# Performance work log

Measured on AMD Instinct MI355X. Metric: run time of the kernel, lower is better.

Reference implementation:

```python
import jax, jax.numpy as jnp
import numpy as np

N = 100000      # nodes
E = 3200000     # edges (avg degree 32)
F_IN = 512
HID = 256
CLS = 64


def _linear_init(k, fan_in, fan_out):
    lim = 1.0 / np.sqrt(fan_in)
    kw, kb = jax.random.split(k)
    W = jax.random.uniform(kw, (fan_in, fan_out), jnp.float32, -lim, lim)
    b = jax.random.uniform(kb, (fan_out,), jnp.float32, -lim, lim)
    return W, b


def setup_inputs() -> dict:
    key = jax.random.key(0)
    ks = jax.random.split(key, 8)
    x = jax.random.normal(ks[0], (N, F_IN), jnp.float32)
    edge_src = jax.random.randint(ks[1], (E,), 0, N, jnp.int32)
    off = jax.random.randint(ks[2], (E,), 1, N, jnp.int32)
    edge_dst = ((edge_src + off) % N).astype(jnp.int32)  # no self loops
    Wm0, bm0 = _linear_init(ks[3], F_IN, HID)
    Wv0, bv0 = _linear_init(ks[4], F_IN, HID)
    Wm1, bm1 = _linear_init(ks[5], HID, CLS)
    Wv1, bv1 = _linear_init(ks[6], HID, CLS)
    sample = jax.random.normal(ks[7], (N, CLS), jnp.float32)
    return dict(x=x, Wm0=Wm0, bm0=bm0, Wv0=Wv0, bv0=bv0,
                Wm1=Wm1, bm1=bm1, Wv1=Wv1, bv1=bv1,
                sample=sample, edge_src=edge_src, edge_dst=edge_dst)


def reference(x, Wm0, bm0, Wv0, bv0, Wm1, bm1, Wv1, bv1, sample, edge_src, edge_dst):
    n = x.shape[0]
    loops = jnp.arange(n, dtype=edge_src.dtype)
    src = jnp.concatenate([edge_src, loops])  # fill_diag(adj, 1.0)
    dst = jnp.concatenate([edge_dst, loops])
    ones = jnp.ones(src.shape[0], x.dtype)
    deg = jax.ops.segment_sum(ones, src, num_segments=n)
    dis = jnp.where(deg > 0, deg ** -0.5, 0.0)   # D^-0.5
    di = jnp.where(deg > 0, 1.0 / deg, 0.0)      # D^-1
    w0 = dis[src] * dis[dst]                      # adj0 = D^-0.5 A D^-0.5
    w1 = di[src] * di[dst]                        # adj1 = D^-1  A D^-1

    def spmm(w, m):  # (adj @ m) with edge weights w
        return jax.ops.segment_sum(w[:, None] * m[dst], src, num_segments=n)

    # layer 0 (initial=True): no aggregation, dropout off (eval)
    mean = jax.nn.elu(x @ Wm0 + bm0)
    var = jax.nn.relu(x @ Wv0 + bv0)
    # layer 1: variance-attention + dual SpMM
    mean = jax.nn.elu(mean @ Wm1 + bm1)
    var = jax.nn.relu(var @ Wv1 + bv1) + 1e-6
    attn = jnp.exp(-var)
    mean = spmm(w0, mean * attn)
    var = spmm(w1, var * attn * attn)

    out = mean + sample * jnp.sqrt(var)
    return jax.nn.log_softmax(out, axis=-1)
```

## Files before the change

### kernel.cpp

```cpp
#include <hip/hip_runtime.h>
#include <cstdint>
#include <cstddef>


typedef _Float16 h8 __attribute__((ext_vector_type(8)));
typedef _Float16 h2 __attribute__((ext_vector_type(2)));
typedef float f32x4 __attribute__((ext_vector_type(4)));
typedef unsigned int uint32;

#define BSHIFT 7
#define NCHUNK 256

static __device__ __forceinline__ float elu_f(float z) {
  return z > 0.f ? z : expm1f(z);
}

static __device__ __forceinline__ void gload16(const void* g, void* l) {
  __builtin_amdgcn_global_load_lds(
      (__attribute__((address_space(1))) void*)g,
      (__attribute__((address_space(3))) void*)l, 16, 0, 0);
}

__global__ __launch_bounds__(256) void hist_k(const int* __restrict__ esrc, int E,
                                              int chunk, int* __restrict__ h, int NB) {
  __shared__ int sh[1024];
  int t = threadIdx.x;
  for (int i = t; i < NB; i += 256) sh[i] = 0;
  __syncthreads();
  int e0 = blockIdx.x * chunk;
  int e1 = min(e0 + chunk, E);
  for (int e = e0 + t; e < e1; e += 256) atomicAdd(&sh[esrc[e] >> BSHIFT], 1);
  __syncthreads();
  for (int i = t; i < NB; i += 256) h[blockIdx.x * NB + i] = sh[i];
}

__global__ __launch_bounds__(256) void btotal_k(const int* __restrict__ h,
                                                int* __restrict__ tot, int NB) {
  int b = blockIdx.x, t = threadIdx.x;
  int v = h[t * NB + b];
#pragma unroll
  for (int off = 32; off; off >>= 1) v += __shfl_xor(v, off, 64);
  __shared__ int sw[4];
  if ((t & 63) == 0) sw[t >> 6] = v;
  __syncthreads();
  if (t == 0) tot[b] = sw[0] + sw[1] + sw[2] + sw[3];
}

__global__ __launch_bounds__(1024) void bscan_k(const int* __restrict__ tot,
                                                int* __restrict__ base, int NB) {
  __shared__ int sh[1024];
  int t = threadIdx.x;
  int v = (t < NB) ? tot[t] : 0;
  sh[t] = v;
  __syncthreads();
  for (int off = 1; off < 1024; off <<= 1) {
    int add = (t >= off) ? sh[t - off] : 0;
    __syncthreads();
    sh[t] += add;
    __syncthreads();
  }
  if (t < NB) base[t] = sh[t] - v;
  if (t == 1023) base[NB] = sh[1023];
}

__global__ __launch_bounds__(256) void boff_k(int* __restrict__ h,
                                              const int* __restrict__ base, int NB) {
  __shared__ int sh[256];
  int b = blockIdx.x, t = threadIdx.x;
  int v = h[t * NB + b];
  sh[t] = v;
  __syncthreads();
  for (int off = 1; off < 256; off <<= 1) {
    int add = (t >= off) ? sh[t - off] : 0;
    __syncthreads();
    sh[t] += add;
    __syncthreads();
  }
  h[t * NB + b] = base[b] + sh[t] - v;
}

__global__ __launch_bounds__(256) void bscatter_k(
    const int* __restrict__ esrc, const int* __restrict__ edst, int E, int chunk,
    const int* __restrict__ h, int2* __restrict__ pairs, int NB) {
  __shared__ int lcur[1024];
  int t = threadIdx.x;
  for (int i = t; i < NB; i += 256) lcur[i] = h[blockIdx.x * NB + i];
  __syncthreads();
  int e0 = blockIdx.x * chunk;
  int e1 = min(e0 + chunk, E);
  for (int e = e0 + t; e < e1; e += 256) {
    int s = esrc[e], d = edst[e];
    int pos = atomicAdd(&lcur[s >> BSHIFT], 1);
    pairs[pos] = make_int2(s, d);
  }
}

__global__ __launch_bounds__(256) void countN_k(
    const int2* __restrict__ pairs, const int* __restrict__ base,
    int* __restrict__ cnt, float2* __restrict__ dd, int n) {
  __shared__ int c128[128];
  int b = blockIdx.x, t = threadIdx.x;
  if (t < 128) c128[t] = 0;
  __syncthreads();
  int lo = base[b], hi = base[b + 1];
  for (int i = lo + t; i < hi; i += 256) atomicAdd(&c128[pairs[i].x & 127], 1);
  __syncthreads();
  if (t < 128) {
    int node = b * 128 + t;
    if (node < n) {
      int c = c128[t];
      cnt[node] = c;
      float d = (float)(c + 1);
      dd[node] = make_float2(rsqrtf(d), 1.f / d);
    }
  }
}

__global__ __launch_bounds__(256) void partC_k(
    const int2* __restrict__ pairs, const int* __restrict__ base,
    const int* __restrict__ rs, int* __restrict__ csr, int n) {
  __shared__ int lcur[128];
  int b = blockIdx.x, t = threadIdx.x;
  if (t < 128) {
    int node = b * 128 + t;
    lcur[t] = (node < n) ? rs[node] : 0;
  }
  __syncthreads();
  int lo = base[b], hi = base[b + 1];
  for (int i = lo + t; i < hi; i += 256) {
    int2 pr = pairs[i];
    int pos = atomicAdd(&lcur[pr.x & 127], 1);
    csr[pos] = pr.y;
  }
}

__global__ void scan1_k(const int* __restrict__ cnt, int* __restrict__ excl,
                        int* __restrict__ bsum, int n) {
  __shared__ int sh[256];
  int t = threadIdx.x, idx = blockIdx.x * 256 + t;
  int v = (idx < n) ? ((cnt[idx] + 3) & ~3) : 0;
  sh[t] = v;
  __syncthreads();
  for (int off = 1; off < 256; off <<= 1) {
    int add = (t >= off) ? sh[t - off] : 0;
    __syncthreads();
    sh[t] += add;
    __syncthreads();
  }
  if (idx < n) excl[idx] = sh[t] - v;
  if (t == 255) bsum[blockIdx.x] = sh[255];
}

__global__ void scan2_k(const int* __restrict__ bsum, int* __restrict__ boff, int nb) {
  __shared__ int sh[512];
  int t = threadIdx.x;
  int v = (t < nb) ? bsum[t] : 0;
  sh[t] = v;
  __syncthreads();
  for (int off = 1; off < 512; off <<= 1) {
    int add = (t >= off) ? sh[t - off] : 0;
    __syncthreads();
    sh[t] += add;
    __syncthreads();
  }
  if (t < nb) boff[t] = sh[t] - v;
}

__global__ void scan3_k(int* __restrict__ excl, const int* __restrict__ boff, int n) {
  int idx = blockIdx.x * 256 + threadIdx.x;
  if (idx < n) excl[idx] += boff[blockIdx.x];
}

__global__ void prep_w_k(const float* __restrict__ Wm0, const float* __restrict__ Wv0,
                         const float* __restrict__ Wm1, const float* __restrict__ Wv1,
                         _Float16* __restrict__ W1t, _Float16* __restrict__ W2t) {
  int idx = blockIdx.x * 256 + threadIdx.x;
  if (idx < 512 * 512) {
    int n = idx >> 9, k = idx & 511;
    float v = (n < 256) ? Wm0[k * 256 + n] : Wv0[k * 256 + (n - 256)];
    W1t[idx] = (_Float16)v;
  }
  if (idx < 128 * 512) {
    int n = idx >> 9, k = idx & 511;
    float v = 0.f;
    if (n < 64) { if (k < 256) v = Wm1[k * 64 + n]; }
    else        { if (k >= 256) v = Wv1[(k - 256) * 64 + (n - 64)]; }
    W2t[idx] = (_Float16)v;
  }
}

__global__ __launch_bounds__(256) void gemm1_k(
    const float* __restrict__ A, const _Float16* __restrict__ Bt,
    const float* __restrict__ b0, const float* __restrict__ b1,
    _Float16* __restrict__ out, int M, int mtiles) {
  __shared__ __align__(16) unsigned char ldsb[49152];

  const int sg = blockIdx.x >> 5, loc = blockIdx.x & 31;
  const int nt = loc >> 3, mtl = loc & 7;
  const int mt = sg * 8 + mtl;
  if (mt >= mtiles) return;
  const int m0 = mt * 128, n0 = nt * 128;
  const int t = threadIdx.x;
  const int lane = t & 63;
  const int wave = t >> 6;
  const int wm = wave >> 1, wn = wave & 1;
  const int lr = lane & 15, quad = lane >> 4;

  const int ra = t >> 3;
  const int asw = ((t & 7) ^ (ra & 7)) << 2;
  const int rb = t >> 2;
  const int bsw = ((t & 3) ^ ((t >> 3) & 3)) << 3;

  f32x4 acc[4][4] = {};

  auto stage = [&](int b, int kt) {
#pragma unroll
    for (int i = 0; i < 4; i++) {
      const float* src = A + (size_t)min(m0 + i * 32 + ra, M - 1) * 512 + kt + asw;
      gload16(src, ldsb + b * 16384 + i * 4096 + t * 16);
    }
#pragma unroll
    for (int i = 0; i < 2; i++) {
      const _Float16* src = Bt + (size_t)(n0 + i * 64 + rb) * 512 + kt + bsw;
      gload16(src, ldsb + 32768 + b * 8192 + i * 4096 + t * 16);
    }
  };

  stage(0, 0);
  __syncthreads();

  int cur = 0;
  const int zA = lr & 7;
  const int zB = (lr >> 1) & 3;
  for (int kt = 0; kt < 512; kt += 32) {
    if (kt + 32 < 512) stage(cur ^ 1, kt + 32);
    const unsigned char* Ab = ldsb + cur * 16384;
    const unsigned char* Bb = ldsb + 32768 + cur * 8192;
    h8 bf[4];
#pragma unroll
    for (int j = 0; j < 4; j++) {
      int row = wn * 64 + j * 16 + lr;
      bf[j] = *(const h8*)(Bb + row * 64 + ((quad ^ zB) << 4));
    }
    h8 af[4];
#pragma unroll
    for (int i = 0; i < 4; i++) {
      int R = wm * 64 + i * 16 + lr;
      const float4 a0 = *(const float4*)(Ab + R * 128 + (((2 * quad) ^ zA) << 4));
      const float4 a1 = *(const float4*)(Ab + R * 128 + (((2 * quad + 1) ^ zA) << 4));
      af[i] = h8{(_Float16)a0.x, (_Float16)a0.y, (_Float16)a0.z, (_Float16)a0.w,
                 (_Float16)a1.x, (_Float16)a1.y, (_Float16)a1.z, (_Float16)a1.w};
    }
#pragma unroll
    for (int i = 0; i < 4; i++)
#pragma unroll
      for (int j = 0; j < 4; j++)
        acc[i][j] = __builtin_amdgcn_mfma_f32_16x16x32_f16(af[i], bf[j], acc[i][j], 0, 0, 0);
    __syncthreads();
    cur ^= 1;
  }

  _Float16* lt = (_Float16*)ldsb;
#pragma unroll
  for (int j = 0; j < 4; j++) {
    int gc = n0 + wn * 64 + j * 16 + lr;
    float bj = (gc < 256) ? b0[gc] : b1[gc - 256];
#pragma unroll
    for (int i = 0; i < 4; i++) {
#pragma unroll
      for (int r = 0; r < 4; r++) {
        float z = acc[i][j][r] + bj;
        float v = (gc < 256) ? elu_f(z) : fmaxf(z, 0.f);
        lt[(wm * 64 + i * 16 + quad * 4 + r) * 136 + wn * 64 + j * 16 + lr] = (_Float16)v;
      }
    }
  }
  __syncthreads();
  {
    const int row = t >> 1, col0 = (t & 1) * 64;
    const int gr = m0 + row;
    if (gr < M) {
      _Float16* dst = out + (size_t)gr * 512 + n0 + col0;
#pragma unroll
      for (int k = 0; k < 8; k++)
        *(h8*)(dst + k * 8) = *(h8*)&lt[row * 136 + col0 + k * 8];
    }
  }
}

__global__ __launch_bounds__(256) void gemm2_k(
    const _Float16* __restrict__ A, const _Float16* __restrict__ Bt,
    const float* __restrict__ bm1, const float* __restrict__ bv1,
    uint32* __restrict__ Mcat, int M, int K) {
  __shared__ _Float16 lds[20480];
  _Float16* As = lds;
  _Float16* Bs = lds + 10240;
  const int m0 = blockIdx.x * 128;
  const int t = threadIdx.x;
  const int lane = t & 63;
  const int wave = t >> 6;
  const int lr = lane & 15, quad = lane >> 4;
  const int trow = t >> 2;
  const int tkc = (t & 3) * 8;

  const size_t arow0 = (size_t)min(m0 + trow, M - 1) * K;
  const size_t arow1 = (size_t)min(m0 + trow + 64, M - 1) * K;
  const size_t brow0 = (size_t)trow * K;
  const size_t brow1 = (size_t)(trow + 64) * K;

  f32x4 acc[2][8] = {};
  h8 pa[2], pb[2];

  pa[0] = *(const h8*)(A + arow0 + tkc);
  pa[1] = *(const h8*)(A + arow1 + tkc);
  pb[0] = *(const h8*)(Bt + brow0 + tkc);
  pb[1] = *(const h8*)(Bt + brow1 + tkc);
  *(h8*)&As[trow * 40 + tkc] = pa[0];
  *(h8*)&As[(trow + 64) * 40 + tkc] = pa[1];
  *(h8*)&Bs[trow * 40 + tkc] = pb[0];
  *(h8*)&Bs[(trow + 64) * 40 + tkc] = pb[1];
  __syncthreads();

  for (int kt = 0; kt < K; kt += 32) {
    const int cur = (kt >> 5) & 1;
    const int curo = cur * 5120;
    const bool more = (kt + 32) < K;
    if (more) {
      pa[0] = *(const h8*)(A + arow0 + kt + 32 + tkc);
      pa[1] = *(const h8*)(A + arow1 + kt + 32 + tkc);
      pb[0] = *(const h8*)(Bt + brow0 + kt + 32 + tkc);
      pb[1] = *(const h8*)(Bt + brow1 + kt + 32 + tkc);
    }
    h8 af[2], bf[8];
#pragma unroll
    for (int i = 0; i < 2; i++)
      af[i] = *(h8*)&As[curo + (wave * 32 + i * 16 + lr) * 40 + quad * 8];
#pragma unroll
    for (int j = 0; j < 8; j++)
      bf[j] = *(h8*)&Bs[curo + (j * 16 + lr) * 40 + quad * 8];
#pragma unroll
    for (int i = 0; i < 2; i++)
#pragma unroll
      for (int j = 0; j < 8; j++)
        acc[i][j] = __builtin_amdgcn_mfma_f32_16x16x32_f16(af[i], bf[j], acc[i][j], 0, 0, 0);
    if (more) {
      const int nxto = (cur ^ 1) * 5120;
      *(h8*)&As[nxto + trow * 40 + tkc] = pa[0];
      *(h8*)&As[nxto + (trow + 64) * 40 + tkc] = pa[1];
      *(h8*)&Bs[nxto + trow * 40 + tkc] = pb[0];
      *(h8*)&Bs[nxto + (trow + 64) * 40 + tkc] = pb[1];
      __syncthreads();
    }
  }

#pragma unroll
  for (int jm = 0; jm < 4; jm++) {
    int c = jm * 16 + lr;
    float bm = bm1[c], bv = bv1[c];
#pragma unroll
    for (int i = 0; i < 2; i++) {
#pragma unroll
      for (int r = 0; r < 4; r++) {
        int gr = m0 + wave * 32 + i * 16 + quad * 4 + r;
        if (gr < M) {
          float zm = acc[i][jm][r] + bm;
          float zv = acc[i][4 + jm][r] + bv;
          float m = elu_f(zm);
          float v = fmaxf(zv, 0.f) + 1e-6f;
          float a = __expf(-v);
          h2 pk;
          pk.x = (_Float16)(m * a);
          pk.y = (_Float16)(v * a * a);
          Mcat[(size_t)gr * 64 + c] = __builtin_bit_cast(uint32, pk);
        }
      }
    }
  }
}

__global__ __launch_bounds__(256) void spmm_final_k(
    const uint32* __restrict__ Mcat, const float2* __restrict__ dd,
    const int* __restrict__ row_start, const int* __restrict__ cnt,
    const int* __restrict__ csr, const float* __restrict__ sample,
    float* __restrict__ out, int n) {
  int wid = threadIdx.x >> 6, lane = threadIdx.x & 63;
  int r = blockIdx.x * 4 + wid;
  if (r >= n) return;
  float2 wr = dd[r];
  h2 self = __builtin_bit_cast(h2, Mcat[(size_t)r * 64 + lane]);
  float Sm = wr.x * (float)self.x;
  float Sv = wr.y * (float)self.y;
  int start = __builtin_amdgcn_readfirstlane(row_start[r]);
  int c = __builtin_amdgcn_readfirstlane(cnt[r]);
  int j = 0;
  for (; j + 4 <= c; j += 4) {
    int4 d4 = *(const int4*)(csr + start + j);
    float2 w0 = dd[d4.x];
    float2 w1 = dd[d4.y];
    float2 w2 = dd[d4.z];
    float2 w3 = dd[d4.w];
    h2 p0 = __builtin_bit_cast(h2, Mcat[(size_t)d4.x * 64 + lane]);
    h2 p1 = __builtin_bit_cast(h2, Mcat[(size_t)d4.y * 64 + lane]);
    h2 p2 = __builtin_bit_cast(h2, Mcat[(size_t)d4.z * 64 + lane]);
    h2 p3 = __builtin_bit_cast(h2, Mcat[(size_t)d4.w * 64 + lane]);
    Sm += w0.x * (float)p0.x; Sv += w0.y * (float)p0.y;
    Sm += w1.x * (float)p1.x; Sv += w1.y * (float)p1.y;
    Sm += w2.x * (float)p2.x; Sv += w2.y * (float)p2.y;
    Sm += w3.x * (float)p3.x; Sv += w3.y * (float)p3.y;
  }
  for (; j < c; j++) {
    int d = csr[start + j];
    float2 w = dd[d];
    h2 p = __builtin_bit_cast(h2, Mcat[(size_t)d * 64 + lane]);
    Sm += w.x * (float)p.x;
    Sv += w.y * (float)p.y;
  }
  float mean = wr.x * Sm;
  float var = wr.y * Sv;
  float o = mean + sample[(size_t)r * 64 + lane] * sqrtf(var);
  float mx = o;
#pragma unroll
  for (int off = 32; off; off >>= 1) mx = fmaxf(mx, __shfl_xor(mx, off, 64));
  float ex = __expf(o - mx);
  float s = ex;
#pragma unroll
  for (int off = 32; off; off >>= 1) s += __shfl_xor(s, off, 64);
  out[(size_t)r * 64 + lane] = o - mx - logf(s);
}

extern "C" void kernel_launch(void* const* d_in, const int* in_sizes, int n_in,
                              void* d_out, int out_size, void* d_ws, size_t ws_size,
                              hipStream_t stream) {
  (void)n_in; (void)out_size; (void)ws_size;
  const float* x    = (const float*)d_in[0];
  const float* Wm0  = (const float*)d_in[1];
  const float* bm0  = (const float*)d_in[2];
  const float* Wv0  = (const float*)d_in[3];
  const float* bv0  = (const float*)d_in[4];
  const float* Wm1  = (const float*)d_in[5];
  const float* bm1  = (const float*)d_in[6];
  const float* Wv1  = (const float*)d_in[7];
  const float* bv1  = (const float*)d_in[8];
  const float* sample = (const float*)d_in[9];
  const int* esrc   = (const int*)d_in[10];
  const int* edst   = (const int*)d_in[11];
  float* out = (float*)d_out;

  const int N = in_sizes[0] / 512;
  const int E = in_sizes[10];
  const int NB = (N + 127) >> BSHIFT;
  const int chunk = (E + NCHUNK - 1) / NCHUNK;

  uint8_t* p = (uint8_t*)d_ws;
  size_t off = 0;
  auto alloc = [&](size_t bytes) -> void* {
    void* r = p + off;
    off += (bytes + 255) & ~(size_t)255;
    return r;
  };
  _Float16* W1t  = (_Float16*)alloc((size_t)512 * 512 * 2);
  _Float16* W2t  = (_Float16*)alloc((size_t)128 * 512 * 2);
  _Float16* Hcat = (_Float16*)alloc((size_t)N * 512 * 2);
  uint32*   Mcat = (uint32*)alloc((size_t)N * 64 * 4);
  int*   cnt    = (int*)alloc((size_t)N * 4);
  float2* dd    = (float2*)alloc((size_t)N * 8);
  int*   rs     = (int*)alloc((size_t)N * 4);
  int*   h      = (int*)alloc((size_t)NCHUNK * NB * 4);
  int*   tot    = (int*)alloc((size_t)(NB + 1) * 4);
  int*   base   = (int*)alloc((size_t)(NB + 1) * 4);
  int*   bsum   = (int*)alloc(2048);
  int*   boff   = (int*)alloc(2048);
  int*   csr    = (int*)alloc((size_t)(E + 4 * N) * 4);
  int2* pairs = (int2*)Hcat;

  const int nbN = (N + 255) / 256;

  prep_w_k<<<(512 * 512 + 255) / 256, 256, 0, stream>>>(Wm0, Wv0, Wm1, Wv1, W1t, W2t);
  hist_k<<<NCHUNK, 256, 0, stream>>>(esrc, E, chunk, h, NB);
  btotal_k<<<NB, 256, 0, stream>>>(h, tot, NB);
  bscan_k<<<1, 1024, 0, stream>>>(tot, base, NB);
  boff_k<<<NB, 256, 0, stream>>>(h, base, NB);
  bscatter_k<<<NCHUNK, 256, 0, stream>>>(esrc, edst, E, chunk, h, pairs, NB);
  countN_k<<<NB, 256, 0, stream>>>(pairs, base, cnt, dd, N);
  scan1_k<<<nbN, 256, 0, stream>>>(cnt, rs, bsum, N);
  scan2_k<<<1, 512, 0, stream>>>(bsum, boff, nbN);
  scan3_k<<<nbN, 256, 0, stream>>>(rs, boff, N);
  partC_k<<<NB, 256, 0, stream>>>(pairs, base, rs, csr, N);

  const int mtiles = (N + 127) / 128;
  const int sgroups = (mtiles + 7) / 8;
  gemm1_k<<<sgroups * 32, 256, 0, stream>>>(x, W1t, bm0, bv0, Hcat, N, mtiles);
  gemm2_k<<<mtiles, 256, 0, stream>>>(Hcat, W2t, bm1, bv1, Mcat, N, 512);
  spmm_final_k<<<(N + 3) / 4, 256, 0, stream>>>(Mcat, dd, rs, cnt, csr, sample, out, N);
}
```

Before: 720.8 us.

## Convert A to fp16 before LDS in gemm1 and prescale Mcat by destination weights

gemm1 now loads fp32 A rows into registers, converts them to fp16 and stores the fp16 tile into LDS. The old path staged fp32 tiles via global_load_lds and converted on every fragment read, so the change halves LDS footprint and traffic for A. The epilogue is split into two halves to fit the smaller 32KB LDS. gemm2 also folds the per-node dd weight into the fp16 Mcat values, so the SpMM no longer gathers dd per edge. The trade-offs are an extra register-staged load path in gemm1 and slightly different fp16 rounding from scaling before quantization.

```diff
diff --git a/kernel.cpp b/kernel.cpp
--- a/kernel.cpp
+++ b/kernel.cpp
@@ -19,6 +19,11 @@
   __builtin_amdgcn_global_load_lds(
       (__attribute__((address_space(1))) void*)g,
       (__attribute__((address_space(3))) void*)l, 16, 0, 0);
+}
+
+static __device__ __forceinline__ h8 cvt8(float4 a, float4 b) {
+  return h8{(_Float16)a.x, (_Float16)a.y, (_Float16)a.z, (_Float16)a.w,
+            (_Float16)b.x, (_Float16)b.y, (_Float16)b.z, (_Float16)b.w};
 }
 
 __global__ __launch_bounds__(256) void hist_k(const int* __restrict__ esrc, int E,
@@ -189,11 +194,11 @@
   }
 }
 
-__global__ __launch_bounds__(256) void gemm1_k(
+__global__ __launch_bounds__(256) void gemm1r_k(
     const float* __restrict__ A, const _Float16* __restrict__ Bt,
     const float* __restrict__ b0, const float* __restrict__ b1,
     _Float16* __restrict__ out, int M, int mtiles) {
-  __shared__ __align__(16) unsigned char ldsb[49152];
+  __shared__ __align__(16) unsigned char ldsb[32768];
 
   const int sg = blockIdx.x >> 5, loc = blockIdx.x & 31;
   const int nt = loc >> 3, mtl = loc & 7;
@@ -206,84 +211,99 @@
   const int wm = wave >> 1, wn = wave & 1;
   const int lr = lane & 15, quad = lane >> 4;
 
-  const int ra = t >> 3;
-  const int asw = ((t & 7) ^ (ra & 7)) << 2;
   const int rb = t >> 2;
-  const int bsw = ((t & 3) ^ ((t >> 3) & 3)) << 3;
+  const int swE = ((t & 3) ^ ((rb >> 1) & 3)) << 3;
+
+  const float* arow0 = A + (size_t)min(m0 + rb, M - 1) * 512;
+  const float* arow1 = A + (size_t)min(m0 + 64 + rb, M - 1) * 512;
 
   f32x4 acc[4][4] = {};
 
-  auto stage = [&](int b, int kt) {
-#pragma unroll
-    for (int i = 0; i < 4; i++) {
-      const float* src = A + (size_t)min(m0 + i * 32 + ra, M - 1) * 512 + kt + asw;
-      gload16(src, ldsb + b * 16384 + i * 4096 + t * 16);
-    }
+  auto stageB = [&](int b, int kt) {
 #pragma unroll
     for (int i = 0; i < 2; i++) {
-      const _Float16* src = Bt + (size_t)(n0 + i * 64 + rb) * 512 + kt + bsw;
-      gload16(src, ldsb + 32768 + b * 8192 + i * 4096 + t * 16);
+      const _Float16* src = Bt + (size_t)(n0 + i * 64 + rb) * 512 + kt + swE;
+      gload16(src, ldsb + b * 16384 + 8192 + i * 4096 + t * 16);
     }
   };
 
-  stage(0, 0);
-  __syncthreads();
-
+  {
+    float4 a00 = ((const float4*)(arow0 + swE))[0];
+    float4 a01 = ((const float4*)(arow0 + swE))[1];
+    float4 a10 = ((const float4*)(arow1 + swE))[0];
+    float4 a11 = ((const float4*)(arow1 + swE))[1];
+    stageB(0, 0);
+    *(h8*)(ldsb + t * 16) = cvt8(a00, a01);
+    *(h8*)(ldsb + 4096 + t * 16) = cvt8(a10, a11);
+  }
+  __syncthreads();
+
+  const int z = (lr >> 1) & 3;
   int cur = 0;
-  const int zA = lr & 7;
-  const int zB = (lr >> 1) & 3;
   for (int kt = 0; kt < 512; kt += 32) {
-    if (kt + 32 < 512) stage(cur ^ 1, kt + 32);
+    const bool more = (kt + 32) < 512;
+    float4 a00, a01, a10, a11;
+    if (more) {
+      const float* s0 = arow0 + kt + 32 + swE;
+      const float* s1 = arow1 + kt + 32 + swE;
+      a00 = ((const float4*)s0)[0]; a01 = ((const float4*)s0)[1];
+      a10 = ((const float4*)s1)[0]; a11 = ((const float4*)s1)[1];
+      stageB(cur ^ 1, kt + 32);
+    }
     const unsigned char* Ab = ldsb + cur * 16384;
-    const unsigned char* Bb = ldsb + 32768 + cur * 8192;
-    h8 bf[4];
-#pragma unroll
-    for (int j = 0; j < 4; j++) {
-      int row = wn * 64 + j * 16 + lr;
-      bf[j] = *(const h8*)(Bb + row * 64 + ((quad ^ zB) << 4));
-    }
-    h8 af[4];
-#pragma unroll
-    for (int i = 0; i < 4; i++) {
-      int R = wm * 64 + i * 16 + lr;
-      const float4 a0 = *(const float4*)(Ab + R * 128 + (((2 * quad) ^ zA) << 4));
-      const float4 a1 = *(const float4*)(Ab + R * 128 + (((2 * quad + 1) ^ zA) << 4));
-      af[i] = h8{(_Float16)a0.x, (_Float16)a0.y, (_Float16)a0.z, (_Float16)a0.w,
-                 (_Float16)a1.x, (_Float16)a1.y, (_Float16)a1.z, (_Float16)a1.w};
-    }
+    const unsigned char* Bb = Ab + 8192;
+    h8 af[4], bf[4];
+#pragma unroll
+    for (int i = 0; i < 4; i++)
+      af[i] = *(const h8*)(Ab + (wm * 64 + i * 16 + lr) * 64 + ((quad ^ z) << 4));
+#pragma unroll
+    for (int j = 0; j < 4; j++)
+      bf[j] = *(const h8*)(Bb + (wn * 64 + j * 16 + lr) * 64 + ((quad ^ z) << 4));
 #pragma unroll
     for (int i = 0; i < 4; i++)
 #pragma unroll
       for (int j = 0; j < 4; j++)
         acc[i][j] = __builtin_amdgcn_mfma_f32_16x16x32_f16(af[i], bf[j], acc[i][j], 0, 0, 0);
+    if (more) {
+      const int nb = cur ^ 1;
+      *(h8*)(ldsb + nb * 16384 + t * 16) = cvt8(a00, a01);
+      *(h8*)(ldsb + nb * 16384 + 4096 + t * 16) = cvt8(a10, a11);
+    }
     __syncthreads();
     cur ^= 1;
   }
 
   _Float16* lt = (_Float16*)ldsb;
 #pragma unroll
-  for (int j = 0; j < 4; j++) {
-    int gc = n0 + wn * 64 + j * 16 + lr;
-    float bj = (gc < 256) ? b0[gc] : b1[gc - 256];
-#pragma unroll
-    for (int i = 0; i < 4; i++) {
-#pragma unroll
-      for (int r = 0; r < 4; r++) {
-        float z = acc[i][j][r] + bj;
-        float v = (gc < 256) ? elu_f(z) : fmaxf(z, 0.f);
-        lt[(wm * 64 + i * 16 + quad * 4 + r) * 136 + wn * 64 + j * 16 + lr] = (_Float16)v;
+  for (int hh = 0; hh < 2; hh++) {
+    __syncthreads();
+    if (wm == hh) {
+#pragma unroll
+      for (int j = 0; j < 4; j++) {
+        int gc = n0 + wn * 64 + j * 16 + lr;
+        float bj = (gc < 256) ? b0[gc] : b1[gc - 256];
+#pragma unroll
+        for (int i = 0; i < 4; i++) {
+#pragma unroll
+          for (int r = 0; r < 4; r++) {
+            float zz = acc[i][j][r] + bj;
+            float v = (gc < 256) ? elu_f(zz) : fmaxf(zz, 0.f);
+            lt[(i * 16 + quad * 4 + r) * 136 + wn * 64 + j * 16 + lr] = (_Float16)v;
+          }
+        }
       }
     }
-  }
-  __syncthreads();
-  {
-    const int row = t >> 1, col0 = (t & 1) * 64;
-    const int gr = m0 + row;
-    if (gr < M) {
-      _Float16* dst = out + (size_t)gr * 512 + n0 + col0;
-#pragma unroll
-      for (int k = 0; k < 8; k++)
-        *(h8*)(dst + k * 8) = *(h8*)&lt[row * 136 + col0 + k * 8];
+    __syncthreads();
+    {
+      const int row = t >> 2, c0 = (t & 3) * 32;
+      const int gr = m0 + hh * 64 + row;
+      if (gr < M) {
+        _Float16* dst = out + (size_t)gr * 512 + n0 + c0;
+        const _Float16* srow = lt + row * 136 + c0;
+#pragma unroll
+        for (int k = 0; k < 4; k++)
+          *(h8*)(dst + k * 8) = *(const h8*)(srow + k * 8);
+      }
     }
   }
 }
@@ -291,7 +311,7 @@
 __global__ __launch_bounds__(256) void gemm2_k(
     const _Float16* __restrict__ A, const _Float16* __restrict__ Bt,
     const float* __restrict__ bm1, const float* __restrict__ bv1,
-    uint32* __restrict__ Mcat, int M, int K) {
+    const float2* __restrict__ dd, uint32* __restrict__ Mcat, int M, int K) {
   __shared__ _Float16 lds[20480];
   _Float16* As = lds;
   _Float16* Bs = lds + 10240;
@@ -353,6 +373,15 @@
     }
   }
 
+  float2 wrow[2][4];
+#pragma unroll
+  for (int i = 0; i < 2; i++)
+#pragma unroll
+    for (int r = 0; r < 4; r++) {
+      int gr = m0 + wave * 32 + i * 16 + quad * 4 + r;
+      wrow[i][r] = (gr < M) ? dd[gr] : make_float2(0.f, 0.f);
+    }
+
 #pragma unroll
   for (int jm = 0; jm < 4; jm++) {
     int c = jm * 16 + lr;
@@ -369,8 +398,8 @@
           float v = fmaxf(zv, 0.f) + 1e-6f;
           float a = __expf(-v);
           h2 pk;
-          pk.x = (_Float16)(m * a);
-          pk.y = (_Float16)(v * a * a);
+          pk.x = (_Float16)(m * a * wrow[i][r].x);
+          pk.y = (_Float16)(v * a * a * wrow[i][r].y);
           Mcat[(size_t)gr * 64 + c] = __builtin_bit_cast(uint32, pk);
         }
       }
@@ -388,32 +417,25 @@
   if (r >= n) return;
   float2 wr = dd[r];
   h2 self = __builtin_bit_cast(h2, Mcat[(size_t)r * 64 + lane]);
-  float Sm = wr.x * (float)self.x;
-  float Sv = wr.y * (float)self.y;
+  float Sm = (float)self.x;
+  float Sv = (float)self.y;
   int start = __builtin_amdgcn_readfirstlane(row_start[r]);
   int c = __builtin_amdgcn_readfirstlane(cnt[r]);
   int j = 0;
   for (; j + 4 <= c; j += 4) {
     int4 d4 = *(const int4*)(csr + start + j);
-    float2 w0 = dd[d4.x];
-    float2 w1 = dd[d4.y];
-    float2 w2 = dd[d4.z];
-    float2 w3 = dd[d4.w];
     h2 p0 = __builtin_bit_cast(h2, Mcat[(size_t)d4.x * 64 + lane]);
     h2 p1 = __builtin_bit_cast(h2, Mcat[(size_t)d4.y * 64 + lane]);
     h2 p2 = __builtin_bit_cast(h2, Mcat[(size_t)d4.z * 64 + lane]);
     h2 p3 = __builtin_bit_cast(h2, Mcat[(size_t)d4.w * 64 + lane]);
-    Sm += w0.x * (float)p0.x; Sv += w0.y * (float)p0.y;
-    Sm += w1.x * (float)p1.x; Sv += w1.y * (float)p1.y;
-    Sm += w2.x * (float)p2.x; Sv += w2.y * (float)p2.y;
-    Sm += w3.x * (float)p3.x; Sv += w3.y * (float)p3.y;
+    Sm += (float)p0.x + (float)p1.x + (float)p2.x + (float)p3.x;
+    Sv += (float)p0.y + (float)p1.y + (float)p2.y + (float)p3.y;
   }
   for (; j < c; j++) {
     int d = csr[start + j];
-    float2 w = dd[d];
     h2 p = __builtin_bit_cast(h2, Mcat[(size_t)d * 64 + lane]);
-    Sm += w.x * (float)p.x;
-    Sv += w.y * (float)p.y;
+    Sm += (float)p.x;
+    Sv += (float)p.y;
   }
   float mean = wr.x * Sm;
   float var = wr.y * Sv;
@@ -489,7 +511,7 @@
 
   const int mtiles = (N + 127) / 128;
   const int sgroups = (mtiles + 7) / 8;
-  gemm1_k<<<sgroups * 32, 256, 0, stream>>>(x, W1t, bm0, bv0, Hcat, N, mtiles);
-  gemm2_k<<<mtiles, 256, 0, stream>>>(Hcat, W2t, bm1, bv1, Mcat, N, 512);
+  gemm1r_k<<<sgroups * 32, 256, 0, stream>>>(x, W1t, bm0, bv0, Hcat, N, mtiles);
+  gemm2_k<<<mtiles, 256, 0, stream>>>(Hcat, W2t, bm1, bv1, dd, Mcat, N, 512);
   spmm_final_k<<<(N + 3) / 4, 256, 0, stream>>>(Mcat, dd, rs, cnt, csr, sample, out, N);
 }
```

Result: slower. 749.7 us (+4.0%).

## Replace bucketed CSR build with global atomics and pre-scale messages by degree

Applied to the files above, without the earlier changes.

Swaps the two-level bucket sort CSR construction (hist/scan/scatter/count/partition kernels) for a direct global-atomic count and scatter. This cuts several kernel launches and one extra pass over an edge-pair buffer, but relies on atomics into global memory and gives a non-deterministic neighbor order within each row. Moves the per-destination degree weights into gemm2's epilogue, so the SpMM no longer gathers dd for every neighbor. The SpMM inner loop is also unrolled to eight neighbors to keep more gathers in flight.

```diff
diff --git a/kernel.cpp b/kernel.cpp
--- a/kernel.cpp
+++ b/kernel.cpp
@@ -8,9 +8,6 @@
 typedef float f32x4 __attribute__((ext_vector_type(4)));
 typedef unsigned int uint32;
 
-#define BSHIFT 7
-#define NCHUNK 256
-
 static __device__ __forceinline__ float elu_f(float z) {
   return z > 0.f ? z : expm1f(z);
 }
@@ -21,124 +18,38 @@
       (__attribute__((address_space(3))) void*)l, 16, 0, 0);
 }
 
-__global__ __launch_bounds__(256) void hist_k(const int* __restrict__ esrc, int E,
-                                              int chunk, int* __restrict__ h, int NB) {
-  __shared__ int sh[1024];
-  int t = threadIdx.x;
-  for (int i = t; i < NB; i += 256) sh[i] = 0;
-  __syncthreads();
-  int e0 = blockIdx.x * chunk;
-  int e1 = min(e0 + chunk, E);
-  for (int e = e0 + t; e < e1; e += 256) atomicAdd(&sh[esrc[e] >> BSHIFT], 1);
-  __syncthreads();
-  for (int i = t; i < NB; i += 256) h[blockIdx.x * NB + i] = sh[i];
-}
-
-__global__ __launch_bounds__(256) void btotal_k(const int* __restrict__ h,
-                                                int* __restrict__ tot, int NB) {
-  int b = blockIdx.x, t = threadIdx.x;
-  int v = h[t * NB + b];
-#pragma unroll
-  for (int off = 32; off; off >>= 1) v += __shfl_xor(v, off, 64);
-  __shared__ int sw[4];
-  if ((t & 63) == 0) sw[t >> 6] = v;
-  __syncthreads();
-  if (t == 0) tot[b] = sw[0] + sw[1] + sw[2] + sw[3];
-}
-
-__global__ __launch_bounds__(1024) void bscan_k(const int* __restrict__ tot,
-                                                int* __restrict__ base, int NB) {
-  __shared__ int sh[1024];
-  int t = threadIdx.x;
-  int v = (t < NB) ? tot[t] : 0;
-  sh[t] = v;
-  __syncthreads();
-  for (int off = 1; off < 1024; off <<= 1) {
-    int add = (t >= off) ? sh[t - off] : 0;
-    __syncthreads();
-    sh[t] += add;
-    __syncthreads();
-  }
-  if (t < NB) base[t] = sh[t] - v;
-  if (t == 1023) base[NB] = sh[1023];
-}
-
-__global__ __launch_bounds__(256) void boff_k(int* __restrict__ h,
-                                              const int* __restrict__ base, int NB) {
-  __shared__ int sh[256];
-  int b = blockIdx.x, t = threadIdx.x;
-  int v = h[t * NB + b];
-  sh[t] = v;
-  __syncthreads();
-  for (int off = 1; off < 256; off <<= 1) {
-    int add = (t >= off) ? sh[t - off] : 0;
-    __syncthreads();
-    sh[t] += add;
-    __syncthreads();
-  }
-  h[t * NB + b] = base[b] + sh[t] - v;
-}
-
-__global__ __launch_bounds__(256) void bscatter_k(
-    const int* __restrict__ esrc, const int* __restrict__ edst, int E, int chunk,
-    const int* __restrict__ h, int2* __restrict__ pairs, int NB) {
-  __shared__ int lcur[1024];
-  int t = threadIdx.x;
-  for (int i = t; i < NB; i += 256) lcur[i] = h[blockIdx.x * NB + i];
-  __syncthreads();
-  int e0 = blockIdx.x * chunk;
-  int e1 = min(e0 + chunk, E);
-  for (int e = e0 + t; e < e1; e += 256) {
-    int s = esrc[e], d = edst[e];
-    int pos = atomicAdd(&lcur[s >> BSHIFT], 1);
-    pairs[pos] = make_int2(s, d);
-  }
-}
-
-__global__ __launch_bounds__(256) void countN_k(
-    const int2* __restrict__ pairs, const int* __restrict__ base,
-    int* __restrict__ cnt, float2* __restrict__ dd, int n) {
-  __shared__ int c128[128];
-  int b = blockIdx.x, t = threadIdx.x;
-  if (t < 128) c128[t] = 0;
-  __syncthreads();
-  int lo = base[b], hi = base[b + 1];
-  for (int i = lo + t; i < hi; i += 256) atomicAdd(&c128[pairs[i].x & 127], 1);
-  __syncthreads();
-  if (t < 128) {
-    int node = b * 128 + t;
-    if (node < n) {
-      int c = c128[t];
-      cnt[node] = c;
-      float d = (float)(c + 1);
-      dd[node] = make_float2(rsqrtf(d), 1.f / d);
-    }
-  }
-}
-
-__global__ __launch_bounds__(256) void partC_k(
-    const int2* __restrict__ pairs, const int* __restrict__ base,
-    const int* __restrict__ rs, int* __restrict__ csr, int n) {
-  __shared__ int lcur[128];
-  int b = blockIdx.x, t = threadIdx.x;
-  if (t < 128) {
-    int node = b * 128 + t;
-    lcur[t] = (node < n) ? rs[node] : 0;
-  }
-  __syncthreads();
-  int lo = base[b], hi = base[b + 1];
-  for (int i = lo + t; i < hi; i += 256) {
-    int2 pr = pairs[i];
-    int pos = atomicAdd(&lcur[pr.x & 127], 1);
-    csr[pos] = pr.y;
+__global__ __launch_bounds__(256) void zero_k(int* __restrict__ cnt, int n) {
+  int idx = blockIdx.x * 256 + threadIdx.x;
+  if (idx < n) cnt[idx] = 0;
+}
+
+__global__ __launch_bounds__(256) void countA_k(const int* __restrict__ esrc, int E,
+                                                int* __restrict__ cnt) {
+  int idx = blockIdx.x * 256 + threadIdx.x;
+  if (idx < E) atomicAdd(&cnt[esrc[idx]], 1);
+}
+
+__global__ __launch_bounds__(256) void scatterA_k(
+    const int* __restrict__ esrc, const int* __restrict__ edst, int E,
+    int* __restrict__ cur, int* __restrict__ csr) {
+  int idx = blockIdx.x * 256 + threadIdx.x;
+  if (idx < E) {
+    int s = esrc[idx];
+    int pos = atomicAdd(&cur[s], 1);
+    csr[pos] = edst[idx];
   }
 }
 
 __global__ void scan1_k(const int* __restrict__ cnt, int* __restrict__ excl,
-                        int* __restrict__ bsum, int n) {
+                        int* __restrict__ bsum, float2* __restrict__ dd, int n) {
   __shared__ int sh[256];
   int t = threadIdx.x, idx = blockIdx.x * 256 + t;
-  int v = (idx < n) ? ((cnt[idx] + 3) & ~3) : 0;
+  int c = (idx < n) ? cnt[idx] : 0;
+  if (idx < n) {
+    float d = (float)(c + 1);
+    dd[idx] = make_float2(rsqrtf(d), 1.f / d);
+  }
+  int v = (c + 3) & ~3;
   sh[t] = v;
   __syncthreads();
   for (int off = 1; off < 256; off <<= 1) {
@@ -166,9 +77,14 @@
   if (t < nb) boff[t] = sh[t] - v;
 }
 
-__global__ void scan3_k(int* __restrict__ excl, const int* __restrict__ boff, int n) {
+__global__ void scan3_k(int* __restrict__ excl, const int* __restrict__ boff,
+                        int* __restrict__ cur, int n) {
   int idx = blockIdx.x * 256 + threadIdx.x;
-  if (idx < n) excl[idx] += boff[blockIdx.x];
+  if (idx < n) {
+    int v = excl[idx] + boff[blockIdx.x];
+    excl[idx] = v;
+    cur[idx] = v;
+  }
 }
 
 __global__ void prep_w_k(const float* __restrict__ Wm0, const float* __restrict__ Wv0,
@@ -189,7 +105,7 @@
   }
 }
 
-__global__ __launch_bounds__(256) void gemm1_k(
+__global__ __launch_bounds__(256) void gemm1f_k(
     const float* __restrict__ A, const _Float16* __restrict__ Bt,
     const float* __restrict__ b0, const float* __restrict__ b1,
     _Float16* __restrict__ out, int M, int mtiles) {
@@ -291,7 +207,7 @@
 __global__ __launch_bounds__(256) void gemm2_k(
     const _Float16* __restrict__ A, const _Float16* __restrict__ Bt,
     const float* __restrict__ bm1, const float* __restrict__ bv1,
-    uint32* __restrict__ Mcat, int M, int K) {
+    const float2* __restrict__ dd, uint32* __restrict__ Mcat, int M, int K) {
   __shared__ _Float16 lds[20480];
   _Float16* As = lds;
   _Float16* Bs = lds + 10240;
@@ -353,6 +269,15 @@
     }
   }
 
+  float2 wrow[2][4];
+#pragma unroll
+  for (int i = 0; i < 2; i++)
+#pragma unroll
+    for (int r = 0; r < 4; r++) {
+      int gr = m0 + wave * 32 + i * 16 + quad * 4 + r;
+      wrow[i][r] = (gr < M) ? dd[gr] : make_float2(0.f, 0.f);
+    }
+
 #pragma unroll
   for (int jm = 0; jm < 4; jm++) {
     int c = jm * 16 + lr;
@@ -369,8 +294,8 @@
           float v = fmaxf(zv, 0.f) + 1e-6f;
           float a = __expf(-v);
           h2 pk;
-          pk.x = (_Float16)(m * a);
-          pk.y = (_Float16)(v * a * a);
+          pk.x = (_Float16)(m * a * wrow[i][r].x);
+          pk.y = (_Float16)(v * a * a * wrow[i][r].y);
           Mcat[(size_t)gr * 64 + c] = __builtin_bit_cast(uint32, pk);
         }
       }
@@ -388,32 +313,42 @@
   if (r >= n) return;
   float2 wr = dd[r];
   h2 self = __builtin_bit_cast(h2, Mcat[(size_t)r * 64 + lane]);
-  float Sm = wr.x * (float)self.x;
-  float Sv = wr.y * (float)self.y;
+  float Sm = (float)self.x;
+  float Sv = (float)self.y;
   int start = __builtin_amdgcn_readfirstlane(row_start[r]);
   int c = __builtin_amdgcn_readfirstlane(cnt[r]);
   int j = 0;
-  for (; j + 4 <= c; j += 4) {
+  for (; j + 8 <= c; j += 8) {
+    int4 da = *(const int4*)(csr + start + j);
+    int4 db = *(const int4*)(csr + start + j + 4);
+    h2 p0 = __builtin_bit_cast(h2, Mcat[(size_t)da.x * 64 + lane]);
+    h2 p1 = __builtin_bit_cast(h2, Mcat[(size_t)da.y * 64 + lane]);
+    h2 p2 = __builtin_bit_cast(h2, Mcat[(size_t)da.z * 64 + lane]);
+    h2 p3 = __builtin_bit_cast(h2, Mcat[(size_t)da.w * 64 + lane]);
+    h2 p4 = __builtin_bit_cast(h2, Mcat[(size_t)db.x * 64 + lane]);
+    h2 p5 = __builtin_bit_cast(h2, Mcat[(size_t)db.y * 64 + lane]);
+    h2 p6 = __builtin_bit_cast(h2, Mcat[(size_t)db.z * 64 + lane]);
+    h2 p7 = __builtin_bit_cast(h2, Mcat[(size_t)db.w * 64 + lane]);
+    Sm += (float)p0.x + (float)p1.x + (float)p2.x + (float)p3.x;
+    Sv += (float)p0.y + (float)p1.y + (float)p2.y + (float)p3.y;
+    Sm += (float)p4.x + (float)p5.x + (float)p6.x + (float)p7.x;
+    Sv += (float)p4.y + (float)p5.y + (float)p6.y + (float)p7.y;
+  }
+  if (j + 4 <= c) {
     int4 d4 = *(const int4*)(csr + start + j);
-    float2 w0 = dd[d4.x];
-    float2 w1 = dd[d4.y];
-    float2 w2 = dd[d4.z];
-    float2 w3 = dd[d4.w];
     h2 p0 = __builtin_bit_cast(h2, Mcat[(size_t)d4.x * 64 + lane]);
     h2 p1 = __builtin_bit_cast(h2, Mcat[(size_t)d4.y * 64 + lane]);
     h2 p2 = __builtin_bit_cast(h2, Mcat[(size_t)d4.z * 64 + lane]);
     h2 p3 = __builtin_bit_cast(h2, Mcat[(size_t)d4.w * 64 + lane]);
-    Sm += w0.x * (float)p0.x; Sv += w0.y * (float)p0.y;
-    Sm += w1.x * (float)p1.x; Sv += w1.y * (float)p1.y;
-    Sm += w2.x * (float)p2.x; Sv += w2.y * (float)p2.y;
-    Sm += w3.x * (float)p3.x; Sv += w3.y * (float)p3.y;
+    Sm += (float)p0.x + (float)p1.x + (float)p2.x + (float)p3.x;
+    Sv += (float)p0.y + (float)p1.y + (float)p2.y + (float)p3.y;
+    j += 4;
   }
   for (; j < c; j++) {
     int d = csr[start + j];
-    float2 w = dd[d];
     h2 p = __builtin_bit_cast(h2, Mcat[(size_t)d * 64 + lane]);
-    Sm += w.x * (float)p.x;
-    Sv += w.y * (float)p.y;
+    Sm += (float)p.x;
+    Sv += (float)p.y;
   }
   float mean = wr.x * Sm;
   float var = wr.y * Sv;
@@ -448,8 +383,6 @@
 
   const int N = in_sizes[0] / 512;
   const int E = in_sizes[10];
-  const int NB = (N + 127) >> BSHIFT;
-  const int chunk = (E + NCHUNK - 1) / NCHUNK;
 
   uint8_t* p = (uint8_t*)d_ws;
   size_t off = 0;
@@ -465,31 +398,25 @@
   int*   cnt    = (int*)alloc((size_t)N * 4);
   float2* dd    = (float2*)alloc((size_t)N * 8);
   int*   rs     = (int*)alloc((size_t)N * 4);
-  int*   h      = (int*)alloc((size_t)NCHUNK * NB * 4);
-  int*   tot    = (int*)alloc((size_t)(NB + 1) * 4);
-  int*   base   = (int*)alloc((size_t)(NB + 1) * 4);
+  int*   cur    = (int*)alloc((size_t)N * 4);
   int*   bsum   = (int*)alloc(2048);
   int*   boff   = (int*)alloc(2048);
   int*   csr    = (int*)alloc((size_t)(E + 4 * N) * 4);
-  int2* pairs = (int2*)Hcat;
 
   const int nbN = (N + 255) / 256;
+  const int nbE = (E + 255) / 256;
 
   prep_w_k<<<(512 * 512 + 255) / 256, 256, 0, stream>>>(Wm0, Wv0, Wm1, Wv1, W1t, W2t);
-  hist_k<<<NCHUNK, 256, 0, stream>>>(esrc, E, chunk, h, NB);
-  btotal_k<<<NB, 256, 0, stream>>>(h, tot, NB);
-  bscan_k<<<1, 1024, 0, stream>>>(tot, base, NB);
-  boff_k<<<NB, 256, 0, stream>>>(h, base, NB);
-  bscatter_k<<<NCHUNK, 256, 0, stream>>>(esrc, edst, E, chunk, h, pairs, NB);
-  countN_k<<<NB, 256, 0, stream>>>(pairs, base, cnt, dd, N);
-  scan1_k<<<nbN, 256, 0, stream>>>(cnt, rs, bsum, N);
+  zero_k<<<nbN, 256, 0, stream>>>(cnt, N);
+  countA_k<<<nbE, 256, 0, stream>>>(esrc, E, cnt);
+  scan1_k<<<nbN, 256, 0, stream>>>(cnt, rs, bsum, dd, N);
   scan2_k<<<1, 512, 0, stream>>>(bsum, boff, nbN);
-  scan3_k<<<nbN, 256, 0, stream>>>(rs, boff, N);
-  partC_k<<<NB, 256, 0, stream>>>(pairs, base, rs, csr, N);
+  scan3_k<<<nbN, 256, 0, stream>>>(rs, boff, cur, N);
+  scatterA_k<<<nbE, 256, 0, stream>>>(esrc, edst, E, cur, csr);
 
   const int mtiles = (N + 127) / 128;
   const int sgroups = (mtiles + 7) / 8;
-  gemm1_k<<<sgroups * 32, 256, 0, stream>>>(x, W1t, bm0, bv0, Hcat, N, mtiles);
-  gemm2_k<<<mtiles, 256, 0, stream>>>(Hcat, W2t, bm1, bv1, Mcat, N, 512);
+  gemm1f_k<<<sgroups * 32, 256, 0, stream>>>(x, W1t, bm0, bv0, Hcat, N, mtiles);
+  gemm2_k<<<mtiles, 256, 0, stream>>>(Hcat, W2t, bm1, bv1, dd, Mcat, N, 512);
   spmm_final_k<<<(N + 3) / 4, 256, 0, stream>>>(Mcat, dd, rs, cnt, csr, sample, out, N);
 }
```

Result: slower. 969.7 us (+34.5%).
